# Kernel optimization log

Hardware: AMD Instinct MI355X
Metric: run time of the kernel (lower is better)

## Reference

```python
import jax, jax.numpy as jnp
import numpy as np
import math

EPS = 1e-07
LOG2PI = math.log(2.0 * math.pi)
ITERS = 3
FINAL_LAMBDA = 0.01


def setup_inputs() -> dict:
    key = jax.random.key(0)
    k1, k2, k3, k4 = jax.random.split(key, 4)
    B, oH, oW, KH, KW, IC, OC, P = 4, 12, 12, 3, 3, 16, 32, 16
    V = jax.random.normal(k1, (B, oH, oW, KH, KW, IC, OC, P), dtype=jnp.float32)
    a = jax.random.uniform(k2, (B, oH, oW, KH, KW, IC), dtype=jnp.float32)
    Beta_u = jax.random.normal(k3, (OC, 1), dtype=jnp.float32)
    Beta_a = jax.random.normal(k4, (OC,), dtype=jnp.float32)
    return {"V": V, "a": a, "Beta_u": Beta_u, "Beta_a": Beta_a,
            "outSize": (B, oH, oW, OC, P), "outCaps": OC}


def reference(V, a, Beta_u, Beta_a, outSize, outCaps):
    # R: [B,oH,oW,KH,KW,inCaps,outCaps]
    R = jnp.full(a.shape + (outCaps,), 1.0 / outCaps, dtype=V.dtype)
    a6 = a[..., None]  # [B,oH,oW,KH,KW,inCaps,1]
    for i in range(ITERS):
        Lambda = FINAL_LAMBDA * (1.0 - 0.95 ** (i + 1))
        Rw = (R * a6)[..., None]  # [...,inCaps,outCaps,1]
        mu_denom = Rw.sum(axis=(3, 4, 5), keepdims=True)  # [B,oH,oW,1,1,1,OC,1]
        mu = (Rw * V).sum(axis=(3, 4, 5), keepdims=True) / (mu_denom + EPS)
        V_mu_sqr = (V - mu) ** 2
        sigma_sqr = (Rw * V_mu_sqr).sum(axis=(3, 4, 5), keepdims=True) / (mu_denom + EPS)
        cost_h = (Beta_u + 0.5 * jnp.log(sigma_sqr)) * mu_denom
        x = Lambda * (Beta_a - cost_h.sum(axis=7))  # [B,oH,oW,1,1,1,OC]
        # F.normalize(x, dim=6): L2-normalize with eps=1e-12 clamp
        norm = jnp.maximum(jnp.sqrt((x * x).sum(axis=6, keepdims=True)), 1e-12)
        a_out = jax.nn.sigmoid(x / norm)
        log_p1 = -0.5 * (LOG2PI + jnp.log(sigma_sqr)).sum(axis=7) + EPS
        log_p2 = -(V_mu_sqr / (2.0 * sigma_sqr + EPS)).sum(axis=7)
        R = jax.nn.softmax(jnp.log(a_out) + log_p1 + log_p2, axis=6)
    mu_out = jnp.squeeze(mu).reshape(outSize)
    sigma_out = jnp.squeeze(sigma_sqr).reshape(outSize)
    return mu_out, jnp.squeeze(a_out), sigma_out
```

## Files before the change

kernel.cpp:

```cpp
#include <hip/hip_runtime.h>

#define NPOS 576
#define KTOT 144
#define NOC 32
#define NP 16
#define OCP 512
#define NCQ 128
#define CHUNK 48
#define RPT 12
#define NCHUNK 3
#define EPSF 1e-7f
#define LOG2PIF 1.83787706640934548356f

__global__ __launch_bounds__(512, 4) void em_routing(
    const float* __restrict__ Vf, const float* __restrict__ Af,
    const float* __restrict__ Bup, const float* __restrict__ Bap,
    float* __restrict__ out)
{
  const int pos = blockIdx.x;
  const int t   = (int)threadIdx.x;
  const int c   = t & 127;
  const int rs  = t >> 7;
  const int oc  = c >> 2;

  __shared__ float sA[KTOT];
  __shared__ float sL[2][CHUNK][NOC];
  __shared__ float sRed[4][NCQ][9];
  __shared__ float sX[NOC];
  __shared__ float sBase[NOC];

  const float4* __restrict__ V4 =
      (const float4*)(Vf + (size_t)pos * (KTOT * OCP));

  if (t < KTOT) sA[t] = Af[pos * KTOT + t];
  const float Bu = Bup[oc];
  const float Ba = Bap[oc];
  __syncthreads();

  float  s0 = 0.f;
  float4 s1 = {0.f,0.f,0.f,0.f}, s2 = {0.f,0.f,0.f,0.f};
  #pragma unroll 12
  for (int r = 0; r < 36; ++r) {
    const int k = rs + 4 * r;
    const float w = sA[k] * (1.0f / 32.0f);
    const float4 v = V4[k * NCQ + c];
    s0 += w;
    s1.x += w * v.x; s1.y += w * v.y; s1.z += w * v.z; s1.w += w * v.w;
    s2.x += w * v.x * v.x; s2.y += w * v.y * v.y;
    s2.z += w * v.z * v.z; s2.w += w * v.w * v.w;
  }

  float4 mu, sig;
  float aout = 0.5f;

  for (int it = 0; it < 3; ++it) {
    const float lam = (it == 0) ? 5e-4f : (it == 1) ? 9.75e-4f : 1.42625e-3f;

    sRed[rs][c][0] = s0;
    sRed[rs][c][1] = s1.x; sRed[rs][c][2] = s1.y;
    sRed[rs][c][3] = s1.z; sRed[rs][c][4] = s1.w;
    sRed[rs][c][5] = s2.x; sRed[rs][c][6] = s2.y;
    sRed[rs][c][7] = s2.z; sRed[rs][c][8] = s2.w;
    __syncthreads();
    {
      float a0 = 0.f, a1 = 0.f, a2 = 0.f, a3 = 0.f, a4 = 0.f,
            a5 = 0.f, a6 = 0.f, a7 = 0.f, a8 = 0.f;
      #pragma unroll
      for (int q = 0; q < 4; ++q) {
        a0 += sRed[q][c][0];
        a1 += sRed[q][c][1]; a2 += sRed[q][c][2];
        a3 += sRed[q][c][3]; a4 += sRed[q][c][4];
        a5 += sRed[q][c][5]; a6 += sRed[q][c][6];
        a7 += sRed[q][c][7]; a8 += sRed[q][c][8];
      }
      s0 = a0;
      s1.x = a1; s1.y = a2; s1.z = a3; s1.w = a4;
      s2.x = a5; s2.y = a6; s2.z = a7; s2.w = a8;
    }

    const float inv = 1.0f / (s0 + EPSF);
    mu.x = s1.x * inv; mu.y = s1.y * inv; mu.z = s1.z * inv; mu.w = s1.w * inv;
    sig.x = fmaxf(s2.x * inv - mu.x * mu.x, 1e-30f);
    sig.y = fmaxf(s2.y * inv - mu.y * mu.y, 1e-30f);
    sig.z = fmaxf(s2.z * inv - mu.z * mu.z, 1e-30f);
    sig.w = fmaxf(s2.w * inv - mu.w * mu.w, 1e-30f);

    float Lown = logf(sig.x) + logf(sig.y) + logf(sig.z) + logf(sig.w);
    float L1 = Lown + __shfl_xor(Lown, 1, 4);
    const float L = L1 + __shfl_xor(L1, 2, 4);

    const float x = lam * (Ba - s0 * (16.0f * Bu + 0.5f * L));
    if (rs == 0 && (c & 3) == 0) sX[oc] = x;
    __syncthreads();
    float ss = 0.f;
    #pragma unroll
    for (int j = 0; j < NOC; ++j) ss += sX[j] * sX[j];
    const float nrm = fmaxf(sqrtf(ss), 1e-12f);
    aout = 1.0f / (1.0f + expf(-x / nrm));

    if (it == 2) break;

    float4 c0q;
    c0q.x = 1.0f / (2.0f * sig.x + EPSF);
    c0q.y = 1.0f / (2.0f * sig.y + EPSF);
    c0q.z = 1.0f / (2.0f * sig.z + EPSF);
    c0q.w = 1.0f / (2.0f * sig.w + EPSF);
    if (rs == 0 && (c & 3) == 0)
      sBase[oc] = logf(aout) + (-0.5f * (16.0f * LOG2PIF + L) + EPSF);
    __syncthreads();

    float  n0 = 0.f;
    float4 n1 = {0.f,0.f,0.f,0.f}, n2 = {0.f,0.f,0.f,0.f};
    for (int ch = 0; ch < NCHUNK; ++ch) {
      const int b = ch & 1;
      const int kbase = ch * CHUNK;
      float4 vloc[RPT];
      #pragma unroll
      for (int r = 0; r < RPT; ++r)
        vloc[r] = V4[(kbase + rs + 4 * r) * NCQ + c];

      #pragma unroll
      for (int r = 0; r < RPT; ++r) {
        const float4 v = vloc[r];
        const float dx = v.x - mu.x, dy = v.y - mu.y,
                    dz = v.z - mu.z, dw = v.w - mu.w;
        float q = dx * dx * c0q.x + dy * dy * c0q.y
                + dz * dz * c0q.z + dw * dw * c0q.w;
        q += __shfl_xor(q, 1, 4);
        q += __shfl_xor(q, 2, 4);
        if ((c & 3) == 0) sL[b][rs + 4 * r][oc] = q;
      }
      __syncthreads();

      #pragma unroll
      for (int j = 0; j < 3; ++j) {
        const int idx = t + 512 * j;
        const int kl = idx >> 5, o = idx & 31;
        const float val = sBase[o] - sL[b][kl][o];
        float mx = val;
        #pragma unroll
        for (int m = 1; m < 32; m <<= 1) mx = fmaxf(mx, __shfl_xor(mx, m, 32));
        const float e = expf(val - mx);
        float sum = e;
        #pragma unroll
        for (int m = 1; m < 32; m <<= 1) sum += __shfl_xor(sum, m, 32);
        sL[b][kl][o] = e * (sA[kbase + kl] / sum);
      }
      __syncthreads();

      #pragma unroll
      for (int r = 0; r < RPT; ++r) {
        const float w = sL[b][rs + 4 * r][oc];
        const float4 v = vloc[r];
        n0 += w;
        n1.x += w * v.x; n1.y += w * v.y; n1.z += w * v.z; n1.w += w * v.w;
        n2.x += w * v.x * v.x; n2.y += w * v.y * v.y;
        n2.z += w * v.z * v.z; n2.w += w * v.w * v.w;
      }
    }
    s0 = n0; s1 = n1; s2 = n2;
  }

  if (rs == 0) {
    float4* __restrict__ out4 = (float4*)out;
    out4[(size_t)pos * NCQ + c]         = mu;
    out4[78336u + (size_t)pos * NCQ + c] = sig;
    if ((c & 3) == 0) out[294912u + (size_t)pos * NOC + oc] = aout;
  }
}

extern "C" void kernel_launch(void* const* d_in, const int* in_sizes, int n_in,
                              void* d_out, int out_size, void* d_ws, size_t ws_size,
                              hipStream_t stream) {
  em_routing<<<NPOS, 512, 0, stream>>>((const float*)d_in[0], (const float*)d_in[1],
                                       (const float*)d_in[2], (const float*)d_in[3],
                                       (float*)d_out);
}
```

Before: 96.43 us.

## Keep V slice register-resident across EM iterations with 1024-thread blocks

Blocks grow to 1024 threads (8 row slots), so each thread holds its 18 float4 V rows in registers, loaded once in the initial pass. The later EM iterations reuse those registers instead of re-reading V from global memory. The chunked double-buffered shared scratch is replaced by one full 144x32 shared array, which cuts the per-iteration barriers from six to two. The cost is 72 registers of V per thread at 1024 threads per block, which lowers occupancy and may force register spills.

```diff
diff --git a/kernel.cpp b/kernel.cpp
--- a/kernel.cpp
+++ b/kernel.cpp
@@ -6,13 +6,12 @@
 #define NP 16
 #define OCP 512
 #define NCQ 128
-#define CHUNK 48
-#define RPT 12
-#define NCHUNK 3
+#define NSLOT 8
+#define RPT 18
 #define EPSF 1e-7f
 #define LOG2PIF 1.83787706640934548356f
 
-__global__ __launch_bounds__(512, 4) void em_routing(
+__global__ __launch_bounds__(1024) void em_routing(
     const float* __restrict__ Vf, const float* __restrict__ Af,
     const float* __restrict__ Bup, const float* __restrict__ Bap,
     float* __restrict__ out)
@@ -24,8 +23,8 @@
   const int oc  = c >> 2;
 
   __shared__ float sA[KTOT];
-  __shared__ float sL[2][CHUNK][NOC];
-  __shared__ float sRed[4][NCQ][9];
+  __shared__ float sL[KTOT][NOC];
+  __shared__ float sRed[NSLOT][NCQ][9];
   __shared__ float sX[NOC];
   __shared__ float sBase[NOC];
 
@@ -37,13 +36,15 @@
   const float Ba = Bap[oc];
   __syncthreads();
 
+  float4 vloc[RPT];
   float  s0 = 0.f;
   float4 s1 = {0.f,0.f,0.f,0.f}, s2 = {0.f,0.f,0.f,0.f};
-  #pragma unroll 12
-  for (int r = 0; r < 36; ++r) {
-    const int k = rs + 4 * r;
+  #pragma unroll
+  for (int r = 0; r < RPT; ++r) {
+    const int k = rs + NSLOT * r;
+    vloc[r] = V4[k * NCQ + c];
     const float w = sA[k] * (1.0f / 32.0f);
-    const float4 v = V4[k * NCQ + c];
+    const float4 v = vloc[r];
     s0 += w;
     s1.x += w * v.x; s1.y += w * v.y; s1.z += w * v.z; s1.w += w * v.w;
     s2.x += w * v.x * v.x; s2.y += w * v.y * v.y;
@@ -63,10 +64,9 @@
     sRed[rs][c][7] = s2.z; sRed[rs][c][8] = s2.w;
     __syncthreads();
     {
-      float a0 = 0.f, a1 = 0.f, a2 = 0.f, a3 = 0.f, a4 = 0.f,
-            a5 = 0.f, a6 = 0.f, a7 = 0.f, a8 = 0.f;
+      float a0=0.f,a1=0.f,a2=0.f,a3=0.f,a4=0.f,a5=0.f,a6=0.f,a7=0.f,a8=0.f;
       #pragma unroll
-      for (int q = 0; q < 4; ++q) {
+      for (int q = 0; q < NSLOT; ++q) {
         a0 += sRed[q][c][0];
         a1 += sRed[q][c][1]; a2 += sRed[q][c][2];
         a3 += sRed[q][c][3]; a4 += sRed[q][c][4];
@@ -109,34 +109,25 @@
       sBase[oc] = logf(aout) + (-0.5f * (16.0f * LOG2PIF + L) + EPSF);
     __syncthreads();
 
-    float  n0 = 0.f;
-    float4 n1 = {0.f,0.f,0.f,0.f}, n2 = {0.f,0.f,0.f,0.f};
-    for (int ch = 0; ch < NCHUNK; ++ch) {
-      const int b = ch & 1;
-      const int kbase = ch * CHUNK;
-      float4 vloc[RPT];
-      #pragma unroll
-      for (int r = 0; r < RPT; ++r)
-        vloc[r] = V4[(kbase + rs + 4 * r) * NCQ + c];
+    #pragma unroll
+    for (int r = 0; r < RPT; ++r) {
+      const float4 v = vloc[r];
+      const float dx = v.x - mu.x, dy = v.y - mu.y,
+                  dz = v.z - mu.z, dw = v.w - mu.w;
+      float q = dx * dx * c0q.x + dy * dy * c0q.y
+              + dz * dz * c0q.z + dw * dw * c0q.w;
+      q += __shfl_xor(q, 1, 4);
+      q += __shfl_xor(q, 2, 4);
+      if ((c & 3) == 0) sL[rs + NSLOT * r][oc] = q;
+    }
+    __syncthreads();
 
-      #pragma unroll
-      for (int r = 0; r < RPT; ++r) {
-        const float4 v = vloc[r];
-        const float dx = v.x - mu.x, dy = v.y - mu.y,
-                    dz = v.z - mu.z, dw = v.w - mu.w;
-        float q = dx * dx * c0q.x + dy * dy * c0q.y
-                + dz * dz * c0q.z + dw * dw * c0q.w;
-        q += __shfl_xor(q, 1, 4);
-        q += __shfl_xor(q, 2, 4);
-        if ((c & 3) == 0) sL[b][rs + 4 * r][oc] = q;
-      }
-      __syncthreads();
-
-      #pragma unroll
-      for (int j = 0; j < 3; ++j) {
-        const int idx = t + 512 * j;
+    #pragma unroll
+    for (int j = 0; j < 5; ++j) {
+      const int idx = t + 1024 * j;
+      if (idx < KTOT * NOC) {
         const int kl = idx >> 5, o = idx & 31;
-        const float val = sBase[o] - sL[b][kl][o];
+        const float val = sBase[o] - sL[kl][o];
         float mx = val;
         #pragma unroll
         for (int m = 1; m < 32; m <<= 1) mx = fmaxf(mx, __shfl_xor(mx, m, 32));
@@ -144,26 +135,28 @@
         float sum = e;
         #pragma unroll
         for (int m = 1; m < 32; m <<= 1) sum += __shfl_xor(sum, m, 32);
-        sL[b][kl][o] = e * (sA[kbase + kl] / sum);
-      }
-      __syncthreads();
-
-      #pragma unroll
-      for (int r = 0; r < RPT; ++r) {
-        const float w = sL[b][rs + 4 * r][oc];
-        const float4 v = vloc[r];
-        n0 += w;
-        n1.x += w * v.x; n1.y += w * v.y; n1.z += w * v.z; n1.w += w * v.w;
-        n2.x += w * v.x * v.x; n2.y += w * v.y * v.y;
-        n2.z += w * v.z * v.z; n2.w += w * v.w * v.w;
+        sL[kl][o] = e * (sA[kl] / sum);
       }
     }
-    s0 = n0; s1 = n1; s2 = n2;
+    __syncthreads();
+
+    s0 = 0.f;
+    s1.x = s1.y = s1.z = s1.w = 0.f;
+    s2.x = s2.y = s2.z = s2.w = 0.f;
+    #pragma unroll
+    for (int r = 0; r < RPT; ++r) {
+      const float w = sL[rs + NSLOT * r][oc];
+      const float4 v = vloc[r];
+      s0 += w;
+      s1.x += w * v.x; s1.y += w * v.y; s1.z += w * v.z; s1.w += w * v.w;
+      s2.x += w * v.x * v.x; s2.y += w * v.y * v.y;
+      s2.z += w * v.z * v.z; s2.w += w * v.w * v.w;
+    }
   }
 
   if (rs == 0) {
     float4* __restrict__ out4 = (float4*)out;
-    out4[(size_t)pos * NCQ + c]         = mu;
+    out4[(size_t)pos * NCQ + c]          = mu;
     out4[78336u + (size_t)pos * NCQ + c] = sig;
     if ((c & 3) == 0) out[294912u + (size_t)pos * NOC + oc] = aout;
   }
@@ -172,7 +165,7 @@
 extern "C" void kernel_launch(void* const* d_in, const int* in_sizes, int n_in,
                               void* d_out, int out_size, void* d_ws, size_t ws_size,
                               hipStream_t stream) {
-  em_routing<<<NPOS, 512, 0, stream>>>((const float*)d_in[0], (const float*)d_in[1],
-                                       (const float*)d_in[2], (const float*)d_in[3],
-                                       (float*)d_out);
+  em_routing<<<NPOS, 1024, 0, stream>>>((const float*)d_in[0], (const float*)d_in[1],
+                                        (const float*)d_in[2], (const float*)d_in[3],
+                                        (float*)d_out);
 }
```

Measured after the change: 179.3 us. +85.9%, slower.
